# Performance work log

Measured on AMD Instinct MI355X. Metric: run time of the kernel, lower is better.

## Reference

```python
import jax, jax.numpy as jnp
import numpy as np

N_FIRMS = 8192
D_IN = 128
EMBED = 128


def setup_inputs() -> dict:
    key = jax.random.key(0)
    k_x, k_q, k_k, k_v, k_h, k_b = jax.random.split(key, 6)
    s_in = 1.0 / np.sqrt(D_IN)
    s_e = 1.0 / np.sqrt(EMBED)
    return {
        "X": jax.random.normal(k_x, (N_FIRMS, D_IN), dtype=jnp.float32),
        # nn.Linear(d_in, embed_dim, bias=False) -> weight shape (embed_dim, d_in)
        "Wq": jax.random.uniform(k_q, (EMBED, D_IN), jnp.float32, -s_in, s_in),
        "Wk": jax.random.uniform(k_k, (EMBED, D_IN), jnp.float32, -s_in, s_in),
        "Wv": jax.random.uniform(k_v, (EMBED, D_IN), jnp.float32, -s_in, s_in),
        # head: Linear(embed_dim, 1, bias=True)
        "head_w": jax.random.uniform(k_h, (1, EMBED), jnp.float32, -s_e, s_e),
        "head_b": jax.random.uniform(k_b, (1,), jnp.float32, -s_e, s_e),
    }


def reference(X, Wq, Wk, Wv, head_w, head_b):
    # Q = X @ Wq^T, K = X @ Wk^T : (N, E)
    Q = X @ Wq.T
    K = X @ Wk.T
    # Linear attention: A = Q K^T (no softmax), shape (N, N)
    A = Q @ K.T
    # dropout p=0.0 -> identity
    V = X @ Wv.T  # (N, E)
    Z = A @ V     # (N, E)
    preds = (Z @ head_w.T + head_b)[:, 0]  # (N,)
    return preds
```

## Files before the change

### kernel.cpp

```cpp
#include <hip/hip_runtime.h>

#define D 128
#define NROWS 8192
#define NBLK 256
#define ROWS_PER_BLK (NROWS / NBLK)

__global__ __launch_bounds__(256) void k2_xa_xty(const float* __restrict__ X,
                                                 const float* __restrict__ Wv,
                                                 const float* __restrict__ head_w,
                                                 float* __restrict__ part) {
    __shared__ float a_s[D];
    __shared__ float red[4][D];
    const int t = threadIdx.x;

    if (t < D) {
        float s0 = 0.f, s1 = 0.f, s2 = 0.f, s3 = 0.f;
#pragma unroll
        for (int e = 0; e < D; e += 4) {
            s0 += Wv[(e + 0) * D + t] * head_w[e + 0];
            s1 += Wv[(e + 1) * D + t] * head_w[e + 1];
            s2 += Wv[(e + 2) * D + t] * head_w[e + 2];
            s3 += Wv[(e + 3) * D + t] * head_w[e + 3];
        }
        a_s[t] = (s0 + s1) + (s2 + s3);
    }
    __syncthreads();

    const int lane = t & 63;
    const int wave = t >> 6;
    const int half = lane >> 5;
    const int l32  = lane & 31;
    const int col  = l32 * 4;
    const float4 a4 = *reinterpret_cast<const float4*>(a_s + col);
    float4 b4 = make_float4(0.f, 0.f, 0.f, 0.f);
    const int rowBase = blockIdx.x * ROWS_PER_BLK + wave * 8 + half;
#pragma unroll
    for (int it = 0; it < 4; ++it) {
        const int row = rowBase + it * 2;
        const float4 x4 = *reinterpret_cast<const float4*>(X + row * D + col);
        float p = x4.x * a4.x + x4.y * a4.y + x4.z * a4.z + x4.w * a4.w;
#pragma unroll
        for (int m = 1; m <= 16; m <<= 1) p += __shfl_xor(p, m, 64);
        b4.x += x4.x * p; b4.y += x4.y * p; b4.z += x4.z * p; b4.w += x4.w * p;
    }
    b4.x += __shfl_xor(b4.x, 32, 64);
    b4.y += __shfl_xor(b4.y, 32, 64);
    b4.z += __shfl_xor(b4.z, 32, 64);
    b4.w += __shfl_xor(b4.w, 32, 64);
    if (half == 0) *reinterpret_cast<float4*>(&red[wave][col]) = b4;
    __syncthreads();
    if (t < D)
        part[blockIdx.x * D + t] = (red[0][t] + red[1][t]) + (red[2][t] + red[3][t]);
}

__global__ __launch_bounds__(256) void k5_fused(const float* __restrict__ part,
                                                const float* __restrict__ Wk,
                                                const float* __restrict__ Wq,
                                                const float* __restrict__ X,
                                                const float* __restrict__ head_b,
                                                float* __restrict__ out) {
    __shared__ float bs[D];
    __shared__ float cs[D];
    __shared__ float w_s[D];
    const int t = threadIdx.x;

    if (t < D) {
        float s0 = 0.f, s1 = 0.f, s2 = 0.f, s3 = 0.f;
#pragma unroll 8
        for (int k = 0; k < NBLK; k += 4) {
            s0 += part[(k + 0) * D + t];
            s1 += part[(k + 1) * D + t];
            s2 += part[(k + 2) * D + t];
            s3 += part[(k + 3) * D + t];
        }
        bs[t] = (s0 + s1) + (s2 + s3);
    }
    __syncthreads();
    if (t < D) {
        float s0 = 0.f, s1 = 0.f, s2 = 0.f, s3 = 0.f;
#pragma unroll
        for (int d = 0; d < D; d += 4) {
            s0 += Wk[t * D + d + 0] * bs[d + 0];
            s1 += Wk[t * D + d + 1] * bs[d + 1];
            s2 += Wk[t * D + d + 2] * bs[d + 2];
            s3 += Wk[t * D + d + 3] * bs[d + 3];
        }
        cs[t] = (s0 + s1) + (s2 + s3);
    }
    __syncthreads();
    if (t < D) {
        float s0 = 0.f, s1 = 0.f, s2 = 0.f, s3 = 0.f;
#pragma unroll
        for (int e = 0; e < D; e += 4) {
            s0 += Wq[(e + 0) * D + t] * cs[e + 0];
            s1 += Wq[(e + 1) * D + t] * cs[e + 1];
            s2 += Wq[(e + 2) * D + t] * cs[e + 2];
            s3 += Wq[(e + 3) * D + t] * cs[e + 3];
        }
        w_s[t] = (s0 + s1) + (s2 + s3);
    }
    __syncthreads();

    const int lane = t & 63;
    const int wave = t >> 6;
    const int half = lane >> 5;
    const int l32  = lane & 31;
    const int col  = l32 * 4;
    const float4 w4 = *reinterpret_cast<const float4*>(w_s + col);
    const float hb = head_b[0];
    const int rowBase = blockIdx.x * ROWS_PER_BLK + wave * 8 + half;
#pragma unroll
    for (int it = 0; it < 4; ++it) {
        const int row = rowBase + it * 2;
        const float4 x4 = *reinterpret_cast<const float4*>(X + row * D + col);
        float p = x4.x * w4.x + x4.y * w4.y + x4.z * w4.z + x4.w * w4.w;
#pragma unroll
        for (int m = 1; m <= 16; m <<= 1) p += __shfl_xor(p, m, 64);
        if (l32 == 0) out[row] = p + hb;
    }
}

extern "C" void kernel_launch(void* const* d_in, const int* in_sizes, int n_in,
                              void* d_out, int out_size, void* d_ws, size_t ws_size,
                              hipStream_t stream) {
    const float* X      = (const float*)d_in[0];
    const float* Wq     = (const float*)d_in[1];
    const float* Wk     = (const float*)d_in[2];
    const float* Wv     = (const float*)d_in[3];
    const float* head_w = (const float*)d_in[4];
    const float* head_b = (const float*)d_in[5];
    float* out = (float*)d_out;

    float* ws_part = (float*)d_ws;

    k2_xa_xty<<<NBLK, 256, 0, stream>>>(X, Wv, head_w, ws_part);
    k5_fused<<<NBLK, 256, 0, stream>>>(ws_part, Wk, Wq, X, head_b, out);
}
```

Baseline: 75.79 us.

## Fuse both kernels into one cooperative launch with grid sync and register-cached X

Merges the two-kernel pipeline into a single cooperative kernel that uses a grid-wide barrier between the partial-sum stage and the final projection stage. X rows are kept in registers across the barrier, so the second pass no longer reloads X from memory. The partial-sum reduction is also split across all 256 threads instead of 128. This removes one kernel launch and the X reload, in exchange for cooperative launch overhead and a grid-sync cost.

```diff
diff --git a/kernel.cpp b/kernel.cpp
--- a/kernel.cpp
+++ b/kernel.cpp
@@ -1,16 +1,27 @@
 #include <hip/hip_runtime.h>
+#include <hip/hip_cooperative_groups.h>
+
+namespace cg = cooperative_groups;
 
 #define D 128
 #define NROWS 8192
 #define NBLK 256
 #define ROWS_PER_BLK (NROWS / NBLK)
 
-__global__ __launch_bounds__(256) void k2_xa_xty(const float* __restrict__ X,
+__global__ __launch_bounds__(256) void fused_all(const float* __restrict__ X,
                                                  const float* __restrict__ Wv,
                                                  const float* __restrict__ head_w,
-                                                 float* __restrict__ part) {
+                                                 const float* __restrict__ Wk,
+                                                 const float* __restrict__ Wq,
+                                                 const float* __restrict__ head_b,
+                                                 float* __restrict__ part,
+                                                 float* __restrict__ out) {
     __shared__ float a_s[D];
     __shared__ float red[4][D];
+    __shared__ float red2[2][D];
+    __shared__ float bs[D];
+    __shared__ float cs[D];
+    __shared__ float w_s[D];
     const int t = threadIdx.x;
 
     if (t < D) {
@@ -32,12 +43,14 @@
     const int l32  = lane & 31;
     const int col  = l32 * 4;
     const float4 a4 = *reinterpret_cast<const float4*>(a_s + col);
+    const int rowBase = blockIdx.x * ROWS_PER_BLK + wave * 8 + half;
+    float4 xs[4];
     float4 b4 = make_float4(0.f, 0.f, 0.f, 0.f);
-    const int rowBase = blockIdx.x * ROWS_PER_BLK + wave * 8 + half;
 #pragma unroll
     for (int it = 0; it < 4; ++it) {
         const int row = rowBase + it * 2;
         const float4 x4 = *reinterpret_cast<const float4*>(X + row * D + col);
+        xs[it] = x4;
         float p = x4.x * a4.x + x4.y * a4.y + x4.z * a4.z + x4.w * a4.w;
 #pragma unroll
         for (int m = 1; m <= 16; m <<= 1) p += __shfl_xor(p, m, 64);
@@ -51,30 +64,24 @@
     __syncthreads();
     if (t < D)
         part[blockIdx.x * D + t] = (red[0][t] + red[1][t]) + (red[2][t] + red[3][t]);
-}
 
-__global__ __launch_bounds__(256) void k5_fused(const float* __restrict__ part,
-                                                const float* __restrict__ Wk,
-                                                const float* __restrict__ Wq,
-                                                const float* __restrict__ X,
-                                                const float* __restrict__ head_b,
-                                                float* __restrict__ out) {
-    __shared__ float bs[D];
-    __shared__ float cs[D];
-    __shared__ float w_s[D];
-    const int t = threadIdx.x;
+    cg::this_grid().sync();
 
-    if (t < D) {
+    {
+        const int d  = t & (D - 1);
+        const int k0 = (t >> 7) * (NBLK / 2);
         float s0 = 0.f, s1 = 0.f, s2 = 0.f, s3 = 0.f;
 #pragma unroll 8
-        for (int k = 0; k < NBLK; k += 4) {
-            s0 += part[(k + 0) * D + t];
-            s1 += part[(k + 1) * D + t];
-            s2 += part[(k + 2) * D + t];
-            s3 += part[(k + 3) * D + t];
+        for (int k = 0; k < NBLK / 2; k += 4) {
+            s0 += part[(k0 + k + 0) * D + d];
+            s1 += part[(k0 + k + 1) * D + d];
+            s2 += part[(k0 + k + 2) * D + d];
+            s3 += part[(k0 + k + 3) * D + d];
         }
-        bs[t] = (s0 + s1) + (s2 + s3);
+        red2[t >> 7][d] = (s0 + s1) + (s2 + s3);
     }
+    __syncthreads();
+    if (t < D) bs[t] = red2[0][t] + red2[1][t];
     __syncthreads();
     if (t < D) {
         float s0 = 0.f, s1 = 0.f, s2 = 0.f, s3 = 0.f;
@@ -101,18 +108,12 @@
     }
     __syncthreads();
 
-    const int lane = t & 63;
-    const int wave = t >> 6;
-    const int half = lane >> 5;
-    const int l32  = lane & 31;
-    const int col  = l32 * 4;
     const float4 w4 = *reinterpret_cast<const float4*>(w_s + col);
     const float hb = head_b[0];
-    const int rowBase = blockIdx.x * ROWS_PER_BLK + wave * 8 + half;
 #pragma unroll
     for (int it = 0; it < 4; ++it) {
         const int row = rowBase + it * 2;
-        const float4 x4 = *reinterpret_cast<const float4*>(X + row * D + col);
+        const float4 x4 = xs[it];
         float p = x4.x * w4.x + x4.y * w4.y + x4.z * w4.z + x4.w * w4.w;
 #pragma unroll
         for (int m = 1; m <= 16; m <<= 1) p += __shfl_xor(p, m, 64);
@@ -130,9 +131,10 @@
     const float* head_w = (const float*)d_in[4];
     const float* head_b = (const float*)d_in[5];
     float* out = (float*)d_out;
+    float* part = (float*)d_ws;
 
-    float* ws_part = (float*)d_ws;
-
-    k2_xa_xty<<<NBLK, 256, 0, stream>>>(X, Wv, head_w, ws_part);
-    k5_fused<<<NBLK, 256, 0, stream>>>(ws_part, Wk, Wq, X, head_b, out);
+    void* args[] = {(void*)&X, (void*)&Wv, (void*)&head_w, (void*)&Wk,
+                    (void*)&Wq, (void*)&head_b, (void*)&part, (void*)&out};
+    hipLaunchCooperativeKernel((void*)fused_all, dim3(NBLK), dim3(256),
+                               args, 0, stream);
 }
```

Measured after the change: 114.2 us. 1.51x slower.

## Compute projected weight vector once in a single-block kernel instead of per block

Applied to the files above, without the earlier changes.

Splits the old fused kernel in two. A one-block kernel now reduces the partial sums and applies Wk and Wq once, and a lightweight kernel does the final X·w row dot products. This removes the redundant per-block 256-way reduction and matrix-vector work that every block used to repeat. The Wv·head_w and Wq matvecs are also restructured to use all 256 threads with float4 loads and a cross-wave reduction. The cost is an extra kernel launch and a serial single-block stage.

```diff
diff --git a/kernel.cpp b/kernel.cpp
--- a/kernel.cpp
+++ b/kernel.cpp
@@ -9,28 +9,34 @@
                                                  const float* __restrict__ Wv,
                                                  const float* __restrict__ head_w,
                                                  float* __restrict__ part) {
+    __shared__ float red[4][D];
     __shared__ float a_s[D];
-    __shared__ float red[4][D];
     const int t = threadIdx.x;
-
-    if (t < D) {
-        float s0 = 0.f, s1 = 0.f, s2 = 0.f, s3 = 0.f;
-#pragma unroll
-        for (int e = 0; e < D; e += 4) {
-            s0 += Wv[(e + 0) * D + t] * head_w[e + 0];
-            s1 += Wv[(e + 1) * D + t] * head_w[e + 1];
-            s2 += Wv[(e + 2) * D + t] * head_w[e + 2];
-            s3 += Wv[(e + 3) * D + t] * head_w[e + 3];
-        }
-        a_s[t] = (s0 + s1) + (s2 + s3);
-    }
-    __syncthreads();
-
     const int lane = t & 63;
     const int wave = t >> 6;
     const int half = lane >> 5;
     const int l32  = lane & 31;
     const int col  = l32 * 4;
+
+    {
+        float4 acc = make_float4(0.f, 0.f, 0.f, 0.f);
+#pragma unroll
+        for (int i = 0; i < 16; ++i) {
+            const int e = wave * 32 + i * 2 + half;
+            const float4 v = *reinterpret_cast<const float4*>(Wv + e * D + col);
+            const float h = head_w[e];
+            acc.x += v.x * h; acc.y += v.y * h; acc.z += v.z * h; acc.w += v.w * h;
+        }
+        acc.x += __shfl_xor(acc.x, 32, 64);
+        acc.y += __shfl_xor(acc.y, 32, 64);
+        acc.z += __shfl_xor(acc.z, 32, 64);
+        acc.w += __shfl_xor(acc.w, 32, 64);
+        if (half == 0) *reinterpret_cast<float4*>(&red[wave][col]) = acc;
+    }
+    __syncthreads();
+    if (t < D) a_s[t] = (red[0][t] + red[1][t]) + (red[2][t] + red[3][t]);
+    __syncthreads();
+
     const float4 a4 = *reinterpret_cast<const float4*>(a_s + col);
     float4 b4 = make_float4(0.f, 0.f, 0.f, 0.f);
     const int rowBase = blockIdx.x * ROWS_PER_BLK + wave * 8 + half;
@@ -53,51 +59,48 @@
         part[blockIdx.x * D + t] = (red[0][t] + red[1][t]) + (red[2][t] + red[3][t]);
 }
 
-__global__ __launch_bounds__(256) void k5_fused(const float* __restrict__ part,
-                                                const float* __restrict__ Wk,
-                                                const float* __restrict__ Wq,
-                                                const float* __restrict__ X,
-                                                const float* __restrict__ head_b,
-                                                float* __restrict__ out) {
+__global__ __launch_bounds__(256) void k3_w(const float* __restrict__ part,
+                                            const float* __restrict__ Wk,
+                                            const float* __restrict__ Wq,
+                                            float* __restrict__ w_out) {
+    __shared__ float4 redp[8][32];
     __shared__ float bs[D];
     __shared__ float cs[D];
-    __shared__ float w_s[D];
+    __shared__ float red[4][D];
     const int t = threadIdx.x;
 
-    if (t < D) {
-        float s0 = 0.f, s1 = 0.f, s2 = 0.f, s3 = 0.f;
-#pragma unroll 8
-        for (int k = 0; k < NBLK; k += 4) {
-            s0 += part[(k + 0) * D + t];
-            s1 += part[(k + 1) * D + t];
-            s2 += part[(k + 2) * D + t];
-            s3 += part[(k + 3) * D + t];
+    {
+        const int ks = t >> 5;
+        const int g  = t & 31;
+        float4 s = make_float4(0.f, 0.f, 0.f, 0.f);
+#pragma unroll 4
+        for (int i = 0; i < 32; ++i) {
+            const float4 v = *reinterpret_cast<const float4*>(part + (ks * 32 + i) * D + g * 4);
+            s.x += v.x; s.y += v.y; s.z += v.z; s.w += v.w;
         }
-        bs[t] = (s0 + s1) + (s2 + s3);
+        redp[ks][g] = s;
     }
     __syncthreads();
-    if (t < D) {
-        float s0 = 0.f, s1 = 0.f, s2 = 0.f, s3 = 0.f;
+    if (t < 32) {
+        float4 s = make_float4(0.f, 0.f, 0.f, 0.f);
 #pragma unroll
-        for (int d = 0; d < D; d += 4) {
-            s0 += Wk[t * D + d + 0] * bs[d + 0];
-            s1 += Wk[t * D + d + 1] * bs[d + 1];
-            s2 += Wk[t * D + d + 2] * bs[d + 2];
-            s3 += Wk[t * D + d + 3] * bs[d + 3];
+        for (int j = 0; j < 8; ++j) {
+            const float4 v = redp[j][t];
+            s.x += v.x; s.y += v.y; s.z += v.z; s.w += v.w;
         }
-        cs[t] = (s0 + s1) + (s2 + s3);
+        *reinterpret_cast<float4*>(bs + t * 4) = s;
     }
     __syncthreads();
+
     if (t < D) {
-        float s0 = 0.f, s1 = 0.f, s2 = 0.f, s3 = 0.f;
-#pragma unroll
-        for (int e = 0; e < D; e += 4) {
-            s0 += Wq[(e + 0) * D + t] * cs[e + 0];
-            s1 += Wq[(e + 1) * D + t] * cs[e + 1];
-            s2 += Wq[(e + 2) * D + t] * cs[e + 2];
-            s3 += Wq[(e + 3) * D + t] * cs[e + 3];
+        float4 s = make_float4(0.f, 0.f, 0.f, 0.f);
+#pragma unroll 4
+        for (int i = 0; i < 32; ++i) {
+            const float4 wv = *reinterpret_cast<const float4*>(Wk + t * D + i * 4);
+            const float4 bv = *reinterpret_cast<const float4*>(bs + i * 4);
+            s.x += wv.x * bv.x; s.y += wv.y * bv.y; s.z += wv.z * bv.z; s.w += wv.w * bv.w;
         }
-        w_s[t] = (s0 + s1) + (s2 + s3);
+        cs[t] = (s.x + s.y) + (s.z + s.w);
     }
     __syncthreads();
 
@@ -106,7 +109,36 @@
     const int half = lane >> 5;
     const int l32  = lane & 31;
     const int col  = l32 * 4;
-    const float4 w4 = *reinterpret_cast<const float4*>(w_s + col);
+    {
+        float4 acc = make_float4(0.f, 0.f, 0.f, 0.f);
+#pragma unroll
+        for (int i = 0; i < 16; ++i) {
+            const int e = wave * 32 + i * 2 + half;
+            const float4 v = *reinterpret_cast<const float4*>(Wq + e * D + col);
+            const float h = cs[e];
+            acc.x += v.x * h; acc.y += v.y * h; acc.z += v.z * h; acc.w += v.w * h;
+        }
+        acc.x += __shfl_xor(acc.x, 32, 64);
+        acc.y += __shfl_xor(acc.y, 32, 64);
+        acc.z += __shfl_xor(acc.z, 32, 64);
+        acc.w += __shfl_xor(acc.w, 32, 64);
+        if (half == 0) *reinterpret_cast<float4*>(&red[wave][col]) = acc;
+    }
+    __syncthreads();
+    if (t < D) w_out[t] = (red[0][t] + red[1][t]) + (red[2][t] + red[3][t]);
+}
+
+__global__ __launch_bounds__(256) void k5_preds(const float* __restrict__ X,
+                                                const float* __restrict__ w_vec,
+                                                const float* __restrict__ head_b,
+                                                float* __restrict__ out) {
+    const int t = threadIdx.x;
+    const int lane = t & 63;
+    const int wave = t >> 6;
+    const int half = lane >> 5;
+    const int l32  = lane & 31;
+    const int col  = l32 * 4;
+    const float4 w4 = *reinterpret_cast<const float4*>(w_vec + col);
     const float hb = head_b[0];
     const int rowBase = blockIdx.x * ROWS_PER_BLK + wave * 8 + half;
 #pragma unroll
@@ -131,8 +163,10 @@
     const float* head_b = (const float*)d_in[5];
     float* out = (float*)d_out;
 
-    float* ws_part = (float*)d_ws;
+    float* part  = (float*)d_ws;
+    float* w_vec = (float*)d_ws + NBLK * D;
 
-    k2_xa_xty<<<NBLK, 256, 0, stream>>>(X, Wv, head_w, ws_part);
-    k5_fused<<<NBLK, 256, 0, stream>>>(ws_part, Wk, Wq, X, head_b, out);
+    k2_xa_xty<<<NBLK, 256, 0, stream>>>(X, Wv, head_w, part);
+    k3_w<<<1, 256, 0, stream>>>(part, Wk, Wq, w_vec);
+    k5_preds<<<NBLK, 256, 0, stream>>>(X, w_vec, head_b, out);
 }
```

Result: no change. 75.45 us (-0.4%).
